# Optimization experiments

Measured on AMD Instinct MI355X. Metric: run time of the kernel, lower is better.

Reference implementation:

```python
import jax, jax.numpy as jnp
import numpy as np

V, L, D, C = 50000, 512, 300, 128
KS = (3, 4, 5)
B = 64


def setup_inputs() -> dict:
    key = jax.random.key(0)
    ks = jax.random.split(key, 12)
    inp = {
        "x": jax.random.randint(ks[0], (B, L), 0, V),
        "embed_w": jax.random.normal(ks[1], (V, D), jnp.float32) * 0.1,
        "conv_w": jax.random.normal(ks[2], (C, D), jnp.float32) * 0.05,
        "conv_b": jax.random.normal(ks[3], (C,), jnp.float32) * 0.05,
        "fc3_w": jax.random.normal(ks[4], (L - 3,), jnp.float32) * 0.04,
        "fc3_b": jax.random.normal(ks[5], (1,), jnp.float32) * 0.04,
        "fc4_w": jax.random.normal(ks[6], (L - 4,), jnp.float32) * 0.04,
        "fc4_b": jax.random.normal(ks[7], (1,), jnp.float32) * 0.04,
        "fc5_w": jax.random.normal(ks[8], (L - 5,), jnp.float32) * 0.04,
        "fc5_b": jax.random.normal(ks[9], (1,), jnp.float32) * 0.04,
        "fc_w": jax.random.normal(ks[10], (C, C * len(KS)), jnp.float32) * 0.05,
        "fc_b": jax.random.normal(ks[11], (C,), jnp.float32) * 0.05,
    }
    return inp


def reference(x, embed_w, conv_w, conv_b, fc3_w, fc3_b, fc4_w, fc4_b,
              fc5_w, fc5_b, fc_w, fc_b):
    # Embedding lookup: [B, L, D]
    emb = embed_w[x]
    # Exclusive prefix sum over the sequence dim (O(L) sliding sums).
    cs = jnp.concatenate(
        [jnp.zeros_like(emb[:, :1]), jnp.cumsum(emb, axis=1)], axis=1)  # [B, L+1, D]
    fcs = ((fc3_w, fc3_b), (fc4_w, fc4_b), (fc5_w, fc5_b))
    outs = []
    for k, (wk, bk) in zip(KS, fcs):
        # Window i sums tokens i..i+k-1; only L-k windows (range(L-k) in original).
        win = cs[:, k:L] - cs[:, :L - k]                      # [B, L-k, D]
        # conv_sim: dot each window-sum against C label vectors (kernel (1, D)).
        sim = jnp.einsum('bld,cd->bcl', win, conv_w) + conv_b[None, :, None]
        # Dropout is identity in eval; fcs[k]: Linear(L-k, 1) shared across channels.
        outs.append(jnp.einsum('bcl,l->bc', sim, wk) + bk)    # [B, C]
    h = jnp.concatenate(outs, axis=1)                          # [B, C*3]
    return h @ fc_w.T + fc_b                                   # [B, C]
```

## Files before the change

kernel.cpp:

```cpp
#include <hip/hip_runtime.h>
#include <stdint.h>

#define BB 64
#define LL 512
#define DD 300
#define CC 128

#define OFF_GRED  (BB * 32 * 3 * DD)
#define OFF_HT    (OFF_GRED + BB * 3 * DD)
#define OFF_SKBK  (OFF_HT + BB * 3 * CC)

__global__ __launch_bounds__(256) void k_gather(
    const int* __restrict__ x, const float* __restrict__ embed,
    const float* __restrict__ w3, const float* __restrict__ w4,
    const float* __restrict__ w5, float* __restrict__ Gpart) {
  const int b = blockIdx.x >> 4;
  const int tc = blockIdx.x & 15;
  const int tid = threadIdx.x;
  const int sub = tid >> 7;
  const int stid = tid & 127;

  __shared__ int sx[32];
  __shared__ float su[3][32];

  if (tid < 32) {
    const int t = tc * 32 + tid;
    sx[tid] = x[b * LL + t];
    const float* ws[3] = {w3, w4, w5};
#pragma unroll
    for (int kk = 0; kk < 3; ++kk) {
      const int k = kk + 3;
      int lo = t - k + 1; if (lo < 0) lo = 0;
      int hi = t; const int lim = LL - k - 1; if (hi > lim) hi = lim;
      float s = 0.f;
      for (int l = lo; l <= hi; ++l) s += ws[kk][l];
      su[kk][tid] = s;
    }
  }
  __syncthreads();

  float a0x = 0.f, a0y = 0.f, a1x = 0.f, a1y = 0.f, a2x = 0.f, a2y = 0.f;
  float c0x = 0.f, c0y = 0.f, c1x = 0.f, c1y = 0.f, c2x = 0.f, c2y = 0.f;
  const bool tail = stid < (DD / 2 - 128);

#pragma unroll 8
  for (int i = 0; i < 16; ++i) {
    const int j = sub * 16 + i;
    const float2* rp = (const float2*)(embed + (size_t)sx[j] * DD);
    const float2 v = rp[stid];
    const float w0 = su[0][j], w1 = su[1][j], w2 = su[2][j];
    a0x += w0 * v.x; a0y += w0 * v.y;
    a1x += w1 * v.x; a1y += w1 * v.y;
    a2x += w2 * v.x; a2y += w2 * v.y;
    if (tail) {
      const float2 v2 = rp[128 + stid];
      c0x += w0 * v2.x; c0y += w0 * v2.y;
      c1x += w1 * v2.x; c1y += w1 * v2.y;
      c2x += w2 * v2.x; c2y += w2 * v2.y;
    }
  }

  const int p = tc * 2 + sub;
  float* Gp = Gpart + (size_t)(b * 32 + p) * (3 * DD);
  const int d0 = 2 * stid;
  Gp[0 * DD + d0] = a0x; Gp[0 * DD + d0 + 1] = a0y;
  Gp[1 * DD + d0] = a1x; Gp[1 * DD + d0 + 1] = a1y;
  Gp[2 * DD + d0] = a2x; Gp[2 * DD + d0 + 1] = a2y;
  if (tail) {
    const int d1 = 2 * (128 + stid);
    Gp[0 * DD + d1] = c0x; Gp[0 * DD + d1 + 1] = c0y;
    Gp[1 * DD + d1] = c1x; Gp[1 * DD + d1 + 1] = c1y;
    Gp[2 * DD + d1] = c2x; Gp[2 * DD + d1 + 1] = c2y;
  }
}

__global__ __launch_bounds__(256) void k_reduce(
    const float* __restrict__ Gpart,
    const float* __restrict__ w3, const float* __restrict__ b3,
    const float* __restrict__ w4, const float* __restrict__ b4,
    const float* __restrict__ w5, const float* __restrict__ b5,
    float* __restrict__ Gred, float* __restrict__ skbk) {
  __shared__ float red[256];
  const int blk = blockIdx.x;
  const int tid = threadIdx.x;

  if (blk < 57) {
    const int idx = blk * 256 + tid;
    if (idx < BB * 225) {
      const int b = idx / 225;
      const int q = idx - b * 225;
      const float4* gp = (const float4*)Gpart + (size_t)b * 32 * 225 + q;
      float4 s0 = gp[0];
      float4 s1 = gp[225];
#pragma unroll
      for (int p = 2; p < 32; p += 2) {
        const float4 v0 = gp[(size_t)p * 225];
        const float4 v1 = gp[(size_t)(p + 1) * 225];
        s0.x += v0.x; s0.y += v0.y; s0.z += v0.z; s0.w += v0.w;
        s1.x += v1.x; s1.y += v1.y; s1.z += v1.z; s1.w += v1.w;
      }
      s0.x += s1.x; s0.y += s1.y; s0.z += s1.z; s0.w += s1.w;
      ((float4*)Gred)[idx] = s0;
    }
  } else {
    const int kk = blk - 57;
    const float* wk = (kk == 0) ? w3 : ((kk == 1) ? w4 : w5);
    const float* bk = (kk == 0) ? b3 : ((kk == 1) ? b4 : b5);
    const int len = LL - (kk + 3);
    float s = (tid < len) ? wk[tid] : 0.f;
    if (tid + 256 < len) s += wk[tid + 256];
    red[tid] = s;
    __syncthreads();
    for (int off = 128; off >= 1; off >>= 1) {
      if (tid < off) red[tid] += red[tid + off];
      __syncthreads();
    }
    if (tid == 0) { skbk[kk] = red[0]; skbk[3 + kk] = bk[0]; }
  }
}

__global__ __launch_bounds__(256) void k_sim(
    const float* __restrict__ Gred, const float* __restrict__ conv_w,
    const float* __restrict__ conv_b, const float* __restrict__ skbk,
    float* __restrict__ hT) {
  const int o = blockIdx.x * 4 + (threadIdx.x >> 6);
  const int lane = threadIdx.x & 63;
  const int b = o / 384;
  const int j = o - b * 384;
  const int kk = j >> 7;
  const int cp = j & 127;

  const float2* cwp = (const float2*)(conv_w + cp * DD);
  const float2* g2 = (const float2*)(Gred + (b * 3 + kk) * DD);

  float acc;
  {
    const float2 v = cwp[lane];
    const float2 g = g2[lane];
    acc = v.x * g.x + v.y * g.y;
  }
  {
    const float2 v = cwp[lane + 64];
    const float2 g = g2[lane + 64];
    acc += v.x * g.x + v.y * g.y;
  }
  if (lane < 22) {
    const float2 v = cwp[lane + 128];
    const float2 g = g2[lane + 128];
    acc += v.x * g.x + v.y * g.y;
  }
#pragma unroll
  for (int off = 32; off >= 1; off >>= 1) acc += __shfl_down(acc, off, 64);
  if (lane == 0) {
    hT[b * (3 * CC) + j] = acc + conv_b[cp] * skbk[kk] + skbk[3 + kk];
  }
}

__global__ __launch_bounds__(256) void k_fc(
    const float* __restrict__ hT, const float* __restrict__ fcw,
    const float* __restrict__ fcb, float* __restrict__ out) {
  const int o = blockIdx.x * 4 + (threadIdx.x >> 6);
  const int lane = threadIdx.x & 63;
  const int b = o >> 7;
  const int c = o & 127;

  const float* fr = fcw + c * (3 * CC);
  const float* hr = hT + b * (3 * CC);
  float acc = 0.f;
#pragma unroll
  for (int s = 0; s < 6; ++s) acc += fr[s * 64 + lane] * hr[s * 64 + lane];
#pragma unroll
  for (int off = 32; off >= 1; off >>= 1) acc += __shfl_down(acc, off, 64);
  if (lane == 0) out[b * CC + c] = acc + fcb[c];
}

extern "C" void kernel_launch(void* const* d_in, const int* in_sizes, int n_in,
                              void* d_out, int out_size, void* d_ws,
                              size_t ws_size, hipStream_t stream) {
  const int* x = (const int*)d_in[0];
  const float* embed = (const float*)d_in[1];
  const float* conv_w = (const float*)d_in[2];
  const float* conv_b = (const float*)d_in[3];
  const float* fc3w = (const float*)d_in[4];
  const float* fc3b = (const float*)d_in[5];
  const float* fc4w = (const float*)d_in[6];
  const float* fc4b = (const float*)d_in[7];
  const float* fc5w = (const float*)d_in[8];
  const float* fc5b = (const float*)d_in[9];
  const float* fcw = (const float*)d_in[10];
  const float* fcb = (const float*)d_in[11];

  float* Gpart = (float*)d_ws;
  float* Gred = Gpart + OFF_GRED;
  float* hT = (float*)d_ws + OFF_HT;
  float* skbk = (float*)d_ws + OFF_SKBK;

  k_gather<<<dim3(BB * 16), dim3(256), 0, stream>>>(x, embed, fc3w, fc4w,
                                                    fc5w, Gpart);
  k_reduce<<<dim3(60), dim3(256), 0, stream>>>(Gpart, fc3w, fc3b, fc4w, fc4b,
                                               fc5w, fc5b, Gred, skbk);
  k_sim<<<dim3(6144), dim3(256), 0, stream>>>(Gred, conv_w, conv_b, skbk, hT);
  k_fc<<<dim3(2048), dim3(256), 0, stream>>>(hT, fcw, fcb, (float*)d_out);
}
```

Baseline: 132.0 us.

## Replace partial-sum reduce kernel with atomics into 4-way split buffers

Removes the separate k_reduce kernel. k_gather now runs with twice as many blocks, each handling 16 tokens, and accumulates its partial weighted embedding sums with atomicAdd into four interleaved slots per batch row. k_sim sums those four slots while loading. The small fc-weight-sum blocks are appended to the gather grid. This trades one kernel launch and the large partial-buffer write and read for a memset, float atomics, and four times the Gred reads in k_sim, and it makes the summation order nondeterministic.

```diff
diff --git a/kernel.cpp b/kernel.cpp
--- a/kernel.cpp
+++ b/kernel.cpp
@@ -6,25 +6,46 @@
 #define DD 300
 #define CC 128
 
-#define OFF_GRED  (BB * 32 * 3 * DD)
-#define OFF_HT    (OFF_GRED + BB * 3 * DD)
-#define OFF_SKBK  (OFF_HT + BB * 3 * CC)
+#define OFF_HT   (BB * 4 * 3 * DD)
+#define OFF_SKBK (OFF_HT + BB * 3 * CC)
 
 __global__ __launch_bounds__(256) void k_gather(
     const int* __restrict__ x, const float* __restrict__ embed,
-    const float* __restrict__ w3, const float* __restrict__ w4,
-    const float* __restrict__ w5, float* __restrict__ Gpart) {
-  const int b = blockIdx.x >> 4;
-  const int tc = blockIdx.x & 15;
+    const float* __restrict__ w3, const float* __restrict__ b3,
+    const float* __restrict__ w4, const float* __restrict__ b4,
+    const float* __restrict__ w5, const float* __restrict__ b5,
+    float* __restrict__ Gred4, float* __restrict__ skbk) {
+  const int blk = blockIdx.x;
   const int tid = threadIdx.x;
+
+  if (blk >= 2048) {
+    __shared__ float red[256];
+    const int kk = blk - 2048;
+    const float* wk = (kk == 0) ? w3 : ((kk == 1) ? w4 : w5);
+    const float* bk = (kk == 0) ? b3 : ((kk == 1) ? b4 : b5);
+    const int len = LL - (kk + 3);
+    float s = (tid < len) ? wk[tid] : 0.f;
+    if (tid + 256 < len) s += wk[tid + 256];
+    red[tid] = s;
+    __syncthreads();
+    for (int off = 128; off >= 1; off >>= 1) {
+      if (tid < off) red[tid] += red[tid + off];
+      __syncthreads();
+    }
+    if (tid == 0) { skbk[kk] = red[0]; skbk[3 + kk] = bk[0]; }
+    return;
+  }
+
+  const int b = blk >> 5;
+  const int tc = blk & 31;
   const int sub = tid >> 7;
   const int stid = tid & 127;
 
-  __shared__ int sx[32];
-  __shared__ float su[3][32];
+  __shared__ int sx[16];
+  __shared__ float su[3][16];
 
-  if (tid < 32) {
-    const int t = tc * 32 + tid;
+  if (tid < 16) {
+    const int t = tc * 16 + tid;
     sx[tid] = x[b * LL + t];
     const float* ws[3] = {w3, w4, w5};
 #pragma unroll
@@ -43,9 +64,9 @@
   float c0x = 0.f, c0y = 0.f, c1x = 0.f, c1y = 0.f, c2x = 0.f, c2y = 0.f;
   const bool tail = stid < (DD / 2 - 128);
 
-#pragma unroll 8
-  for (int i = 0; i < 16; ++i) {
-    const int j = sub * 16 + i;
+#pragma unroll
+  for (int i = 0; i < 8; ++i) {
+    const int j = sub * 8 + i;
     const float2* rp = (const float2*)(embed + (size_t)sx[j] * DD);
     const float2 v = rp[stid];
     const float w0 = su[0][j], w1 = su[1][j], w2 = su[2][j];
@@ -60,67 +81,21 @@
     }
   }
 
-  const int p = tc * 2 + sub;
-  float* Gp = Gpart + (size_t)(b * 32 + p) * (3 * DD);
+  float* Gp = Gred4 + (size_t)((b * 4 + (tc & 3)) * 3) * DD;
   const int d0 = 2 * stid;
-  Gp[0 * DD + d0] = a0x; Gp[0 * DD + d0 + 1] = a0y;
-  Gp[1 * DD + d0] = a1x; Gp[1 * DD + d0 + 1] = a1y;
-  Gp[2 * DD + d0] = a2x; Gp[2 * DD + d0 + 1] = a2y;
+  atomicAdd(&Gp[0 * DD + d0], a0x); atomicAdd(&Gp[0 * DD + d0 + 1], a0y);
+  atomicAdd(&Gp[1 * DD + d0], a1x); atomicAdd(&Gp[1 * DD + d0 + 1], a1y);
+  atomicAdd(&Gp[2 * DD + d0], a2x); atomicAdd(&Gp[2 * DD + d0 + 1], a2y);
   if (tail) {
     const int d1 = 2 * (128 + stid);
-    Gp[0 * DD + d1] = c0x; Gp[0 * DD + d1 + 1] = c0y;
-    Gp[1 * DD + d1] = c1x; Gp[1 * DD + d1 + 1] = c1y;
-    Gp[2 * DD + d1] = c2x; Gp[2 * DD + d1 + 1] = c2y;
-  }
-}
-
-__global__ __launch_bounds__(256) void k_reduce(
-    const float* __restrict__ Gpart,
-    const float* __restrict__ w3, const float* __restrict__ b3,
-    const float* __restrict__ w4, const float* __restrict__ b4,
-    const float* __restrict__ w5, const float* __restrict__ b5,
-    float* __restrict__ Gred, float* __restrict__ skbk) {
-  __shared__ float red[256];
-  const int blk = blockIdx.x;
-  const int tid = threadIdx.x;
-
-  if (blk < 57) {
-    const int idx = blk * 256 + tid;
-    if (idx < BB * 225) {
-      const int b = idx / 225;
-      const int q = idx - b * 225;
-      const float4* gp = (const float4*)Gpart + (size_t)b * 32 * 225 + q;
-      float4 s0 = gp[0];
-      float4 s1 = gp[225];
-#pragma unroll
-      for (int p = 2; p < 32; p += 2) {
-        const float4 v0 = gp[(size_t)p * 225];
-        const float4 v1 = gp[(size_t)(p + 1) * 225];
-        s0.x += v0.x; s0.y += v0.y; s0.z += v0.z; s0.w += v0.w;
-        s1.x += v1.x; s1.y += v1.y; s1.z += v1.z; s1.w += v1.w;
-      }
-      s0.x += s1.x; s0.y += s1.y; s0.z += s1.z; s0.w += s1.w;
-      ((float4*)Gred)[idx] = s0;
-    }
-  } else {
-    const int kk = blk - 57;
-    const float* wk = (kk == 0) ? w3 : ((kk == 1) ? w4 : w5);
-    const float* bk = (kk == 0) ? b3 : ((kk == 1) ? b4 : b5);
-    const int len = LL - (kk + 3);
-    float s = (tid < len) ? wk[tid] : 0.f;
-    if (tid + 256 < len) s += wk[tid + 256];
-    red[tid] = s;
-    __syncthreads();
-    for (int off = 128; off >= 1; off >>= 1) {
-      if (tid < off) red[tid] += red[tid + off];
-      __syncthreads();
-    }
-    if (tid == 0) { skbk[kk] = red[0]; skbk[3 + kk] = bk[0]; }
+    atomicAdd(&Gp[0 * DD + d1], c0x); atomicAdd(&Gp[0 * DD + d1 + 1], c0y);
+    atomicAdd(&Gp[1 * DD + d1], c1x); atomicAdd(&Gp[1 * DD + d1 + 1], c1y);
+    atomicAdd(&Gp[2 * DD + d1], c2x); atomicAdd(&Gp[2 * DD + d1 + 1], c2y);
   }
 }
 
 __global__ __launch_bounds__(256) void k_sim(
-    const float* __restrict__ Gred, const float* __restrict__ conv_w,
+    const float* __restrict__ Gred4, const float* __restrict__ conv_w,
     const float* __restrict__ conv_b, const float* __restrict__ skbk,
     float* __restrict__ hT) {
   const int o = blockIdx.x * 4 + (threadIdx.x >> 6);
@@ -131,23 +106,22 @@
   const int cp = j & 127;
 
   const float2* cwp = (const float2*)(conv_w + cp * DD);
-  const float2* g2 = (const float2*)(Gred + (b * 3 + kk) * DD);
+  const float2* g0 = (const float2*)(Gred4 + (size_t)b * 4 * 3 * DD + kk * DD);
 
-  float acc;
-  {
-    const float2 v = cwp[lane];
-    const float2 g = g2[lane];
-    acc = v.x * g.x + v.y * g.y;
-  }
-  {
-    const float2 v = cwp[lane + 64];
-    const float2 g = g2[lane + 64];
-    acc += v.x * g.x + v.y * g.y;
-  }
-  if (lane < 22) {
-    const float2 v = cwp[lane + 128];
-    const float2 g = g2[lane + 128];
-    acc += v.x * g.x + v.y * g.y;
+  float acc = 0.f;
+#pragma unroll
+  for (int seg = 0; seg < 3; ++seg) {
+    const int idx = lane + seg * 64;
+    if (seg < 2 || lane < 22) {
+      const float2 v = cwp[idx];
+      const float2 ga = g0[idx];
+      const float2 gb = g0[450 + idx];
+      const float2 gc = g0[900 + idx];
+      const float2 gd = g0[1350 + idx];
+      const float gx = (ga.x + gb.x) + (gc.x + gd.x);
+      const float gy = (ga.y + gb.y) + (gc.y + gd.y);
+      acc += v.x * gx + v.y * gy;
+    }
   }
 #pragma unroll
   for (int off = 32; off >= 1; off >>= 1) acc += __shfl_down(acc, off, 64);
@@ -190,15 +164,13 @@
   const float* fcw = (const float*)d_in[10];
   const float* fcb = (const float*)d_in[11];
 
-  float* Gpart = (float*)d_ws;
-  float* Gred = Gpart + OFF_GRED;
+  float* Gred4 = (float*)d_ws;
   float* hT = (float*)d_ws + OFF_HT;
   float* skbk = (float*)d_ws + OFF_SKBK;
 
-  k_gather<<<dim3(BB * 16), dim3(256), 0, stream>>>(x, embed, fc3w, fc4w,
-                                                    fc5w, Gpart);
-  k_reduce<<<dim3(60), dim3(256), 0, stream>>>(Gpart, fc3w, fc3b, fc4w, fc4b,
-                                               fc5w, fc5b, Gred, skbk);
-  k_sim<<<dim3(6144), dim3(256), 0, stream>>>(Gred, conv_w, conv_b, skbk, hT);
+  hipMemsetAsync(Gred4, 0, (size_t)BB * 4 * 3 * DD * sizeof(float), stream);
+  k_gather<<<dim3(2048 + 3), dim3(256), 0, stream>>>(
+      x, embed, fc3w, fc3b, fc4w, fc4b, fc5w, fc5b, Gred4, skbk);
+  k_sim<<<dim3(6144), dim3(256), 0, stream>>>(Gred4, conv_w, conv_b, skbk, hT);
   k_fc<<<dim3(2048), dim3(256), 0, stream>>>(hT, fcw, fcb, (float*)d_out);
 }
```

Measured after the change: 162.1 us. 22.8% more time.
